# Kernel tuning notes

Hardware: AMD Instinct MI355X
Metric: run time of the kernel (lower is better)

Reference implementation:

```python
import jax, jax.numpy as jnp
import numpy as np

B, T, H = 4096, 200, 64
NU, NI, NC = 100000, 1000000, 1000
AU_HID = 36
EPS = 1e-8


def dice(x, alpha):
    # Dice activation: p = sigmoid(batchnorm(x)); out = p*x + (1-p)*alpha*x
    axes = tuple(range(x.ndim - 1))
    m = jnp.mean(x, axis=axes, keepdims=True)
    v = jnp.var(x, axis=axes, keepdims=True)
    p = jax.nn.sigmoid((x - m) * jax.lax.rsqrt(v + EPS))
    return p * x + (1.0 - p) * alpha * x


def setup_inputs() -> dict:
    key = jax.random.key(0)
    ks = jax.random.split(key, 18)
    s = 0.02
    n = lambda k, shp: (jax.random.normal(k, shp, dtype=jnp.float32) * s)
    return {
        "user": jax.random.randint(ks[0], (B,), 0, NU),
        "hist": jax.random.randint(ks[1], (B, T), 0, NI),
        "item": jax.random.randint(ks[2], (B,), 0, NI),
        "cate": jax.random.randint(ks[3], (B,), 0, NC),
        "U": n(ks[4], (NU, H)),
        "I": n(ks[5], (NI, H)),
        "C": n(ks[6], (NC, H)),
        "au_W1": n(ks[7], (4 * H, AU_HID)),
        "au_b1": jnp.zeros((AU_HID,), jnp.float32),
        "au_a1": jnp.zeros((AU_HID,), jnp.float32),
        "au_W2": n(ks[8], (AU_HID, 1)),
        "au_b2": jnp.zeros((1,), jnp.float32),
        "W1": n(ks[9], (4 * H, 80)),
        "b1": jnp.zeros((80,), jnp.float32),
        "a1": jnp.zeros((80,), jnp.float32),
        "W2": n(ks[10], (80, 40)),
        "b2": jnp.zeros((40,), jnp.float32),
        "a2": jnp.zeros((40,), jnp.float32),
        "W3": n(ks[11], (40, 2)),
        "b3": jnp.zeros((2,), jnp.float32),
    }


def reference(user, hist, item, cate, U, I, C,
              au_W1, au_b1, au_a1, au_W2, au_b2,
              W1, b1, a1, W2, b2, a2, W3, b3):
    ue = U[user]            # [B,H]
    ie = I[item]            # [B,H]
    ce = C[cate]            # [B,H]
    he = I[hist]            # [B,T,H] history item embeddings (vectorized over the time loop)
    ieb = jnp.broadcast_to(ie[:, None, :], he.shape)
    # ActivationUnit: concat(hist, item, hist-item, hist*item) -> Linear -> Dice -> Linear(->1)
    au_in = jnp.concatenate([he, ieb, he - ieb, he * ieb], axis=-1)  # [B,T,4H]
    h1 = dice(au_in @ au_W1 + au_b1, au_a1)                          # [B,T,36]
    w = h1 @ au_W2 + au_b2                                           # [B,T,1]
    # weighted-sum pooling over history (original detaches via numpy round-trip)
    cur = jax.lax.stop_gradient(jnp.sum(w * he, axis=1))             # [B,H]
    x = jnp.concatenate([ue, ie, ce, cur], axis=-1)                  # [B,4H]
    x = dice(x @ W1 + b1, a1)
    x = dice(x @ W2 + b2, a2)
    return x @ W3 + b3                                               # [B,2]
```

## Files before the change

### kernel.cpp

```cpp
#include <hip/hip_runtime.h>
#include <math.h>

#define BB 4096
#define TT 200
#define NT (BB*TT)
#define NSPLIT 2
#define RPB 100
#define GEMM_BLOCKS (BB*NSPLIT)

typedef __attribute__((ext_vector_type(8))) __bf16 bf16x8;
typedef __attribute__((ext_vector_type(4))) float f32x4;
typedef __attribute__((ext_vector_type(4))) _Float16 f16x4;

static __device__ __forceinline__ unsigned short f2b(float f) {
  __bf16 b = (__bf16)f;
  return __builtin_bit_cast(unsigned short, b);
}

__global__ __launch_bounds__(256) void k_prep(
    const int* __restrict__ item, const float* __restrict__ Itab,
    const float* __restrict__ auW1, const float* __restrict__ auB1,
    const float* __restrict__ W1, float* __restrict__ TBuf,
    float* __restrict__ W1T) {
  const int blk = blockIdx.x, tid = threadIdx.x;
  if (blk >= BB) {
    int j = blk - BB;
    W1T[j * 256 + tid] = W1[tid * 80 + j];
    return;
  }
  __shared__ float sIe[64];
  if (tid < 64) sIe[tid] = Itab[(size_t)item[blk] * 64 + tid];
  __syncthreads();
  if (tid < 36) {
    const float* Wb_ = auW1 + 64 * 36;
    const float* Wc = auW1 + 128 * 36;
    float a = auB1[tid];
    for (int k = 0; k < 64; ++k)
      a += sIe[k] * (Wb_[k * 36 + tid] - Wc[k * 36 + tid]);
    TBuf[blk * 36 + tid] = a;
  }
}

__global__ __launch_bounds__(256, 4) void k_gemm1(
    const int* __restrict__ hist, const int* __restrict__ item,
    const float* __restrict__ Itab, const float* __restrict__ auW1,
    const float* __restrict__ TBuf, float* __restrict__ PART,
    _Float16* __restrict__ Xb) {
  const int blk = blockIdx.x, tid = threadIdx.x;
  const int b = blk >> 1, half = blk & 1, t0 = half * RPB;
  const int wv = tid >> 6, l = tid & 63;
  const int lr = l & 15, lq = l >> 4;
  __shared__ __align__(16) unsigned short sHe[112 * 72];
  __shared__ __align__(16) unsigned short sWBT[48 * 72];
  __shared__ float sR1[192], sR2[192];

  const float ie_reg = Itab[(size_t)item[b] * 64 + l];

  const int* hp = hist + b * TT + t0;
  int rowi[7];
#pragma unroll
  for (int it = 0; it < 7; ++it) {
    int i = tid + it * 256;
    int ic = i < 1600 ? i : 1599;
    rowi[it] = hp[ic >> 4];
  }
  float4 v[7];
#pragma unroll
  for (int it = 0; it < 7; ++it) {
    int i = tid + it * 256;
    int ic = i < 1600 ? i : 1599;
    v[it] = ((const float4*)(Itab + (size_t)rowi[it] * 64))[ic & 15];
  }
#pragma unroll
  for (int it = 0; it < 7; ++it) {
    int i = tid + it * 256;
    if (i < 1600) {
      ushort4 u;
      u.x = f2b(v[it].x); u.y = f2b(v[it].y);
      u.z = f2b(v[it].z); u.w = f2b(v[it].w);
      *(ushort4*)(sHe + (i >> 4) * 72 + (i & 15) * 4) = u;
    }
  }
  for (int i = tid; i < 12 * 18; i += 256) {
    int r = RPB + i / 18, c = i - (i / 18) * 18;
    *(ushort4*)(sHe + r * 72 + c * 4) = (ushort4){0, 0, 0, 0};
  }
  {
    const float* Wc = auW1 + 128 * 36;
    const float* Wd = auW1 + 192 * 36;
#pragma unroll
    for (int it = 0; it < 12; ++it) {
      int i = tid + it * 256;
      int k = i / 48, n = i - (i / 48) * 48;
      float w = 0.f;
      if (n < 36) {
        int idx = k * 36 + n;
        float iek = __shfl(ie_reg, k, 64);
        w = (auW1[idx] + Wc[idx]) + iek * Wd[idx];
      }
      sWBT[n * 72 + k] = f2b(w);
    }
  }
  float tb3[3];
#pragma unroll
  for (int nt = 0; nt < 3; ++nt) {
    int j = nt * 16 + lr;
    tb3[nt] = (j < 36) ? TBuf[b * 36 + j] : 0.f;
  }
  __syncthreads();

  bf16x8 bfr[3][2];
#pragma unroll
  for (int nt = 0; nt < 3; ++nt)
#pragma unroll
    for (int kh = 0; kh < 2; ++kh)
      bfr[nt][kh] = *reinterpret_cast<const bf16x8*>(
          sWBT + (nt * 16 + lr) * 72 + kh * 32 + lq * 8);

  f32x4 acc[2][3];
#pragma unroll
  for (int mi = 0; mi < 2; ++mi)
#pragma unroll
    for (int nt = 0; nt < 3; ++nt) acc[mi][nt] = (f32x4){0.f, 0.f, 0.f, 0.f};

#pragma unroll
  for (int mi = 0; mi < 2; ++mi) {
    const int mt = wv + mi * 4;
    if (mt <= 6) {
      const unsigned short* ap = sHe + (mt * 16 + lr) * 72 + lq * 8;
      bf16x8 a0 = *reinterpret_cast<const bf16x8*>(ap);
      bf16x8 a1 = *reinterpret_cast<const bf16x8*>(ap + 32);
#pragma unroll
      for (int nt = 0; nt < 3; ++nt) {
        acc[mi][nt] = __builtin_amdgcn_mfma_f32_16x16x32_bf16(
            a0, bfr[nt][0], acc[mi][nt], 0, 0, 0);
        acc[mi][nt] = __builtin_amdgcn_mfma_f32_16x16x32_bf16(
            a1, bfr[nt][1], acc[mi][nt], 0, 0, 0);
      }
    }
  }

  __syncthreads();
  _Float16* sXs = (_Float16*)sHe;

  float s1[3] = {0.f, 0.f, 0.f}, s2[3] = {0.f, 0.f, 0.f};
#pragma unroll
  for (int mi = 0; mi < 2; ++mi) {
    const int mt = wv + mi * 4;
    if (mt <= 6) {
#pragma unroll
      for (int q = 0; q < 4; ++q) {
        const int t = mt * 16 + lq * 4 + q;
        if (t < RPB) {
#pragma unroll
          for (int nt = 0; nt < 3; ++nt) {
            const int j = nt * 16 + lr;
            float x = acc[mi][nt][q] + tb3[nt];
            if (j < 36) {
              s1[nt] += x;
              s2[nt] = fmaf(x, x, s2[nt]);
              sXs[t * 36 + j] = (_Float16)x;
            }
          }
        }
      }
    }
  }
#pragma unroll
  for (int nt = 0; nt < 3; ++nt) {
    float a = s1[nt], c = s2[nt];
    a += __shfl_xor(a, 16, 64); a += __shfl_xor(a, 32, 64);
    c += __shfl_xor(c, 16, 64); c += __shfl_xor(c, 32, 64);
    if (l < 16) {
      sR1[wv * 48 + nt * 16 + l] = a;
      sR2[wv * 48 + nt * 16 + l] = c;
    }
  }
  __syncthreads();
  if (tid < 36) {
    float a = sR1[tid] + sR1[48 + tid] + sR1[96 + tid] + sR1[144 + tid];
    float c = sR2[tid] + sR2[48 + tid] + sR2[96 + tid] + sR2[144 + tid];
    PART[blk * 72 + tid] = a;
    PART[blk * 72 + 36 + tid] = c;
  }
  {
    const uint4* src = (const uint4*)sXs;
    uint4* dst = (uint4*)(Xb + (size_t)b * 7200 + t0 * 36);
    if (tid < 225) {
      dst[tid] = src[tid];
      dst[tid + 225] = src[tid + 225];
    }
  }
}

__global__ __launch_bounds__(256) void k_aust(const float* __restrict__ PART,
                                              float* __restrict__ AUST) {
  int ch = blockIdx.x, tid = threadIdx.x;
  float s1 = 0.f, s2 = 0.f;
  for (int blk = tid; blk < GEMM_BLOCKS; blk += 256) {
    s1 += PART[blk * 72 + ch];
    s2 += PART[blk * 72 + 36 + ch];
  }
  __shared__ float r1[256], r2[256];
  r1[tid] = s1;
  r2[tid] = s2;
  __syncthreads();
  for (int off = 128; off > 0; off >>= 1) {
    if (tid < off) { r1[tid] += r1[tid + off]; r2[tid] += r2[tid + off]; }
    __syncthreads();
  }
  if (tid == 0) {
    float m = r1[0] / (float)NT;
    float var = r2[0] / (float)NT - m * m;
    AUST[ch] = m;
    AUST[36 + ch] = 1.0f / sqrtf(var + 1e-8f);
  }
}

__global__ __launch_bounds__(256) void k_att(
    const int* __restrict__ hist, const int* __restrict__ user,
    const int* __restrict__ item, const int* __restrict__ cate,
    const float* __restrict__ Itab, const float* __restrict__ Utab,
    const float* __restrict__ Ctab, const _Float16* __restrict__ Xb,
    const float* __restrict__ AUST, const float* __restrict__ auA1,
    const float* __restrict__ auW2, const float* __restrict__ auB2,
    const float* __restrict__ W1T, const float* __restrict__ b1,
    float* __restrict__ Y1) {
  const int b = blockIdx.x, tid = threadIdx.x;
  __shared__ float sW[TT];
  __shared__ int sRows[TT];
  __shared__ float sD[144];
  __shared__ float sPart[256];
  __shared__ float sX[256];
  if (tid < TT) sRows[tid] = hist[b * TT + tid];
  if (tid >= 208 && tid < 208 + 36) sD[tid - 208] = AUST[tid - 208];
  else if (tid < 36) sD[36 + tid] = AUST[36 + tid];
  else if (tid >= 64 && tid < 100) sD[72 + (tid - 64)] = auA1[tid - 64];
  else if (tid >= 128 && tid < 164) sD[108 + (tid - 128)] = auW2[tid - 128];
  __syncthreads();
  if (tid < TT) {
    const f16x4* xr = (const f16x4*)(Xb + (size_t)b * 7200 + tid * 36);
    float w = auB2[0];
#pragma unroll
    for (int p = 0; p < 9; ++p) {
      f16x4 pr = xr[p];
#pragma unroll
      for (int h = 0; h < 4; ++h) {
        int j = 4 * p + h;
        float x = (float)pr[h];
        float xh = (x - sD[j]) * sD[36 + j];
        float pp = 1.0f / (1.0f + __expf(-xh));
        float al = sD[72 + j];
        w = fmaf(x * (al + pp * (1.0f - al)), sD[108 + j], w);
      }
    }
    sW[tid] = w;
  }
  __syncthreads();
  {
    const int l = tid & 63, wv = tid >> 6;
    const int t0 = wv * 50;
    float c0 = 0.f, c1 = 0.f, c2 = 0.f, c3 = 0.f;
#pragma unroll
    for (int g = 0; g < 12; ++g) {
      int u = t0 + g * 4;
      c0 = fmaf(sW[u + 0], Itab[(size_t)sRows[u + 0] * 64 + l], c0);
      c1 = fmaf(sW[u + 1], Itab[(size_t)sRows[u + 1] * 64 + l], c1);
      c2 = fmaf(sW[u + 2], Itab[(size_t)sRows[u + 2] * 64 + l], c2);
      c3 = fmaf(sW[u + 3], Itab[(size_t)sRows[u + 3] * 64 + l], c3);
    }
    c0 = fmaf(sW[t0 + 48], Itab[(size_t)sRows[t0 + 48] * 64 + l], c0);
    c1 = fmaf(sW[t0 + 49], Itab[(size_t)sRows[t0 + 49] * 64 + l], c1);
    sPart[tid] = (c0 + c1) + (c2 + c3);
  }
  __syncthreads();
  if (tid < 64) {
    float cur = sPart[tid] + sPart[64 + tid] + sPart[128 + tid] + sPart[192 + tid];
    sX[tid] = Utab[(size_t)user[b] * 64 + tid];
    sX[64 + tid] = Itab[(size_t)item[b] * 64 + tid];
    sX[128 + tid] = Ctab[(size_t)cate[b] * 64 + tid];
    sX[192 + tid] = cur;
  }
  __syncthreads();
  if (tid < 80) {
    float a = b1[tid];
    const float4* wt = (const float4*)(W1T + tid * 256);
#pragma unroll 8
    for (int kq = 0; kq < 64; ++kq) {
      float4 w4 = wt[kq];
      a = fmaf(sX[kq * 4 + 0], w4.x, a);
      a = fmaf(sX[kq * 4 + 1], w4.y, a);
      a = fmaf(sX[kq * 4 + 2], w4.z, a);
      a = fmaf(sX[kq * 4 + 3], w4.w, a);
    }
    Y1[b * 80 + tid] = a;
  }
}

__global__ __launch_bounds__(256) void k_colstats(const float* __restrict__ src,
                                                  int nch, float* __restrict__ st) {
  int ch = blockIdx.x, tid = threadIdx.x;
  float s1 = 0.f, s2 = 0.f;
  for (int r = tid; r < BB; r += 256) {
    float v = src[r * nch + ch];
    s1 += v;
    s2 += v * v;
  }
  __shared__ float r1[256], r2[256];
  r1[tid] = s1;
  r2[tid] = s2;
  __syncthreads();
  for (int off = 128; off > 0; off >>= 1) {
    if (tid < off) { r1[tid] += r1[tid + off]; r2[tid] += r2[tid + off]; }
    __syncthreads();
  }
  if (tid == 0) {
    float m = r1[0] / (float)BB;
    float var = r2[0] / (float)BB - m * m;
    st[ch] = m;
    st[nch + ch] = 1.0f / sqrtf(var + 1e-8f);
  }
}

__global__ __launch_bounds__(128) void k_mlp2(const float* __restrict__ Y1,
                                              const float* __restrict__ ST80,
                                              const float* __restrict__ a1,
                                              const float* __restrict__ W2,
                                              const float* __restrict__ b2,
                                              float* __restrict__ Y2) {
  int b = blockIdx.x, tid = threadIdx.x;
  __shared__ float sY[80];
  if (tid < 80) {
    float x = Y1[b * 80 + tid];
    float xh = (x - ST80[tid]) * ST80[80 + tid];
    float p = 1.0f / (1.0f + expf(-xh));
    sY[tid] = p * x + (1.0f - p) * a1[tid] * x;
  }
  __syncthreads();
  if (tid < 40) {
    float a = b2[tid];
    for (int k = 0; k < 80; ++k) a += sY[k] * W2[k * 40 + tid];
    Y2[b * 40 + tid] = a;
  }
}

__global__ __launch_bounds__(64) void k_mlp3(const float* __restrict__ Y2,
                                             const float* __restrict__ ST40,
                                             const float* __restrict__ a2,
                                             const float* __restrict__ W3,
                                             const float* __restrict__ b3,
                                             float* __restrict__ out) {
  int b = blockIdx.x, tid = threadIdx.x;
  __shared__ float sY[40];
  if (tid < 40) {
    float x = Y2[b * 40 + tid];
    float xh = (x - ST40[tid]) * ST40[40 + tid];
    float p = 1.0f / (1.0f + expf(-xh));
    sY[tid] = p * x + (1.0f - p) * a2[tid] * x;
  }
  __syncthreads();
  if (tid < 2) {
    float a = b3[tid];
    for (int k = 0; k < 40; ++k) a += sY[k] * W3[k * 2 + tid];
    out[b * 2 + tid] = a;
  }
}

extern "C" void kernel_launch(void* const* d_in, const int* in_sizes, int n_in,
                              void* d_out, int out_size, void* d_ws, size_t ws_size,
                              hipStream_t stream) {
  const int* user = (const int*)d_in[0];
  const int* hist = (const int*)d_in[1];
  const int* item = (const int*)d_in[2];
  const int* cate = (const int*)d_in[3];
  const float* Utab = (const float*)d_in[4];
  const float* Itab = (const float*)d_in[5];
  const float* Ctab = (const float*)d_in[6];
  const float* auW1 = (const float*)d_in[7];
  const float* auB1 = (const float*)d_in[8];
  const float* auA1 = (const float*)d_in[9];
  const float* auW2 = (const float*)d_in[10];
  const float* auB2 = (const float*)d_in[11];
  const float* W1 = (const float*)d_in[12];
  const float* b1 = (const float*)d_in[13];
  const float* a1 = (const float*)d_in[14];
  const float* W2 = (const float*)d_in[15];
  const float* b2 = (const float*)d_in[16];
  const float* a2 = (const float*)d_in[17];
  const float* W3 = (const float*)d_in[18];
  const float* b3 = (const float*)d_in[19];
  float* out = (float*)d_out;

  float* ws = (float*)d_ws;
  float* TBuf = ws;
  float* PART = TBuf + BB * 36;
  float* AUST = PART + GEMM_BLOCKS * 72;
  float* Y1 = AUST + 72;
  float* ST80 = Y1 + BB * 80;
  float* Y2 = ST80 + 160;
  float* ST40 = Y2 + BB * 40;
  float* W1T = ST40 + 80;
  _Float16* Xb = (_Float16*)(W1T + 80 * 256);

  k_prep<<<BB + 80, 256, 0, stream>>>(item, Itab, auW1, auB1, W1, TBuf, W1T);
  k_gemm1<<<GEMM_BLOCKS, 256, 0, stream>>>(hist, item, Itab, auW1, TBuf,
                                           PART, Xb);
  k_aust<<<36, 256, 0, stream>>>(PART, AUST);
  k_att<<<BB, 256, 0, stream>>>(hist, user, item, cate, Itab, Utab, Ctab, Xb,
                                AUST, auA1, auW2, auB2, W1T, b1, Y1);
  k_colstats<<<80, 256, 0, stream>>>(Y1, 80, ST80);
  k_mlp2<<<BB, 128, 0, stream>>>(Y1, ST80, a1, W2, b2, Y2);
  k_colstats<<<40, 256, 0, stream>>>(Y2, 40, ST40);
  k_mlp3<<<BB, 64, 0, stream>>>(Y2, ST40, a2, W3, b3, out);
}
```

Before: 189.1 us.

## Process a full 200-step history per block in the activation-unit GEMM

k_gemm1 now handles all 200 history rows of one batch element per block instead of splitting them across two blocks. This halves the number of blocks and removes the duplicated per-block setup: building the item-dependent weight matrix in shared memory, loading the item embedding, and writing partial statistics, which also halves k_aust's reduction input. In exchange, each block uses more shared memory and registers (13 gathers in flight, 4x3 accumulators), and launch bounds drop to 3 blocks per CU, which may reduce occupancy and latency hiding for the gather-heavy load.

```diff
diff --git a/kernel.cpp b/kernel.cpp
--- a/kernel.cpp
+++ b/kernel.cpp
@@ -4,9 +4,6 @@
 #define BB 4096
 #define TT 200
 #define NT (BB*TT)
-#define NSPLIT 2
-#define RPB 100
-#define GEMM_BLOCKS (BB*NSPLIT)
 
 typedef __attribute__((ext_vector_type(8))) __bf16 bf16x8;
 typedef __attribute__((ext_vector_type(4))) float f32x4;
@@ -41,48 +38,47 @@
   }
 }
 
-__global__ __launch_bounds__(256, 4) void k_gemm1(
+__global__ __launch_bounds__(256, 3) void k_gemm1(
     const int* __restrict__ hist, const int* __restrict__ item,
     const float* __restrict__ Itab, const float* __restrict__ auW1,
     const float* __restrict__ TBuf, float* __restrict__ PART,
     _Float16* __restrict__ Xb) {
-  const int blk = blockIdx.x, tid = threadIdx.x;
-  const int b = blk >> 1, half = blk & 1, t0 = half * RPB;
+  const int b = blockIdx.x, tid = threadIdx.x;
   const int wv = tid >> 6, l = tid & 63;
   const int lr = l & 15, lq = l >> 4;
-  __shared__ __align__(16) unsigned short sHe[112 * 72];
+  __shared__ __align__(16) unsigned short sHe[208 * 72];
   __shared__ __align__(16) unsigned short sWBT[48 * 72];
   __shared__ float sR1[192], sR2[192];
 
   const float ie_reg = Itab[(size_t)item[b] * 64 + l];
 
-  const int* hp = hist + b * TT + t0;
-  int rowi[7];
-#pragma unroll
-  for (int it = 0; it < 7; ++it) {
+  const int* hp = hist + b * TT;
+  int rowi[13];
+#pragma unroll
+  for (int it = 0; it < 13; ++it) {
     int i = tid + it * 256;
-    int ic = i < 1600 ? i : 1599;
+    int ic = i < 3200 ? i : 3199;
     rowi[it] = hp[ic >> 4];
   }
-  float4 v[7];
-#pragma unroll
-  for (int it = 0; it < 7; ++it) {
+  float4 v[13];
+#pragma unroll
+  for (int it = 0; it < 13; ++it) {
     int i = tid + it * 256;
-    int ic = i < 1600 ? i : 1599;
+    int ic = i < 3200 ? i : 3199;
     v[it] = ((const float4*)(Itab + (size_t)rowi[it] * 64))[ic & 15];
   }
 #pragma unroll
-  for (int it = 0; it < 7; ++it) {
+  for (int it = 0; it < 13; ++it) {
     int i = tid + it * 256;
-    if (i < 1600) {
+    if (i < 3200) {
       ushort4 u;
       u.x = f2b(v[it].x); u.y = f2b(v[it].y);
       u.z = f2b(v[it].z); u.w = f2b(v[it].w);
       *(ushort4*)(sHe + (i >> 4) * 72 + (i & 15) * 4) = u;
     }
   }
-  for (int i = tid; i < 12 * 18; i += 256) {
-    int r = RPB + i / 18, c = i - (i / 18) * 18;
+  for (int i = tid; i < 8 * 18; i += 256) {
+    int r = TT + i / 18, c = i - (i / 18) * 18;
     *(ushort4*)(sHe + r * 72 + c * 4) = (ushort4){0, 0, 0, 0};
   }
   {
@@ -117,16 +113,16 @@
       bfr[nt][kh] = *reinterpret_cast<const bf16x8*>(
           sWBT + (nt * 16 + lr) * 72 + kh * 32 + lq * 8);
 
-  f32x4 acc[2][3];
-#pragma unroll
-  for (int mi = 0; mi < 2; ++mi)
+  f32x4 acc[4][3];
+#pragma unroll
+  for (int mi = 0; mi < 4; ++mi)
 #pragma unroll
     for (int nt = 0; nt < 3; ++nt) acc[mi][nt] = (f32x4){0.f, 0.f, 0.f, 0.f};
 
 #pragma unroll
-  for (int mi = 0; mi < 2; ++mi) {
+  for (int mi = 0; mi < 4; ++mi) {
     const int mt = wv + mi * 4;
-    if (mt <= 6) {
+    if (mt <= 12) {
       const unsigned short* ap = sHe + (mt * 16 + lr) * 72 + lq * 8;
       bf16x8 a0 = *reinterpret_cast<const bf16x8*>(ap);
       bf16x8 a1 = *reinterpret_cast<const bf16x8*>(ap + 32);
@@ -145,13 +141,13 @@
 
   float s1[3] = {0.f, 0.f, 0.f}, s2[3] = {0.f, 0.f, 0.f};
 #pragma unroll
-  for (int mi = 0; mi < 2; ++mi) {
+  for (int mi = 0; mi < 4; ++mi) {
     const int mt = wv + mi * 4;
-    if (mt <= 6) {
+    if (mt <= 12) {
 #pragma unroll
       for (int q = 0; q < 4; ++q) {
         const int t = mt * 16 + lq * 4 + q;
-        if (t < RPB) {
+        if (t < TT) {
 #pragma unroll
           for (int nt = 0; nt < 3; ++nt) {
             const int j = nt * 16 + lr;
@@ -180,15 +176,16 @@
   if (tid < 36) {
     float a = sR1[tid] + sR1[48 + tid] + sR1[96 + tid] + sR1[144 + tid];
     float c = sR2[tid] + sR2[48 + tid] + sR2[96 + tid] + sR2[144 + tid];
-    PART[blk * 72 + tid] = a;
-    PART[blk * 72 + 36 + tid] = c;
+    PART[b * 72 + tid] = a;
+    PART[b * 72 + 36 + tid] = c;
   }
   {
     const uint4* src = (const uint4*)sXs;
-    uint4* dst = (uint4*)(Xb + (size_t)b * 7200 + t0 * 36);
-    if (tid < 225) {
-      dst[tid] = src[tid];
-      dst[tid + 225] = src[tid + 225];
+    uint4* dst = (uint4*)(Xb + (size_t)b * 7200);
+#pragma unroll
+    for (int it = 0; it < 4; ++it) {
+      int i = tid + it * 256;
+      if (i < 900) dst[i] = src[i];
     }
   }
 }
@@ -197,7 +194,7 @@
                                               float* __restrict__ AUST) {
   int ch = blockIdx.x, tid = threadIdx.x;
   float s1 = 0.f, s2 = 0.f;
-  for (int blk = tid; blk < GEMM_BLOCKS; blk += 256) {
+  for (int blk = tid; blk < BB; blk += 256) {
     s1 += PART[blk * 72 + ch];
     s2 += PART[blk * 72 + 36 + ch];
   }
@@ -394,7 +391,7 @@
   float* ws = (float*)d_ws;
   float* TBuf = ws;
   float* PART = TBuf + BB * 36;
-  float* AUST = PART + GEMM_BLOCKS * 72;
+  float* AUST = PART + BB * 72;
   float* Y1 = AUST + 72;
   float* ST80 = Y1 + BB * 80;
   float* Y2 = ST80 + 160;
@@ -403,8 +400,7 @@
   _Float16* Xb = (_Float16*)(W1T + 80 * 256);
 
   k_prep<<<BB + 80, 256, 0, stream>>>(item, Itab, auW1, auB1, W1, TBuf, W1T);
-  k_gemm1<<<GEMM_BLOCKS, 256, 0, stream>>>(hist, item, Itab, auW1, TBuf,
-                                           PART, Xb);
+  k_gemm1<<<BB, 256, 0, stream>>>(hist, item, Itab, auW1, TBuf, PART, Xb);
   k_aust<<<36, 256, 0, stream>>>(PART, AUST);
   k_att<<<BB, 256, 0, stream>>>(hist, user, item, cate, Itab, Utab, Ctab, Xb,
                                 AUST, auA1, auW2, auB2, W1T, b1, Y1);
```

New measurement: 178.6 us (median of 2 runs). -5.5%, faster.
